# Kernel optimization log

Hardware: AMD Instinct MI355X
Metric: run time of the kernel (lower is better)

## Reference

```python
import jax, jax.numpy as jnp
import numpy as np

B, S, E, H = 4, 2048, 1024, 16
D = E // H  # d_k = 64
NEG = -1000000000.0  # matches torch masked_fill constant


def setup_inputs() -> dict:
    rk = jax.random.key(0)
    kq, kk, kv, km = jax.random.split(rk, 4)
    query = jax.random.normal(kq, (B, S, E), dtype=jnp.float32)
    key = jax.random.normal(kk, (B, S, E), dtype=jnp.float32)
    value = jax.random.normal(kv, (B, S, E), dtype=jnp.float32)
    mask = jax.random.randint(km, (B, S, S), 0, 2, dtype=jnp.int32)
    return {"query": query, "key": key, "value": value, "mask": mask}


def _split_heads(x):
    # (B, S, E) -> (B, H, S, D)
    return x.reshape(B, S, H, D).transpose(0, 2, 1, 3)


def reference(query, key, value, mask):
    q = _split_heads(query)
    k = _split_heads(key)
    v = _split_heads(value)
    scale = np.float32(1.0 / np.sqrt(D))
    scores = jnp.einsum('bhqd,bhkd->bhqk', q, k) * scale  # (B,H,S,S)
    scores = jnp.where(mask[:, None, :, :] == 0, jnp.float32(NEG), scores)
    weights = jax.nn.softmax(scores, axis=-1)
    attn = jnp.einsum('bhqk,bhkd->bhqd', weights, v)  # (B,H,S,D)
    concat = attn.transpose(0, 2, 1, 3).reshape(B, S, E)
    return concat
```

## Files before the change

### kernel.cpp

```cpp
#include <hip/hip_runtime.h>
#include <hip/hip_bf16.h>
#include <math.h>

constexpr int B = 4, S = 2048, E = 1024, H = 16, D = 64;
constexpr float NEGF = -1000000000.0f;
constexpr float KSCALE = 0.125f * 1.44269504f;

typedef __attribute__((ext_vector_type(8))) short short8;
typedef __attribute__((ext_vector_type(16))) float f32x16;

__device__ inline unsigned pk2(float a, float b) {
    unsigned ua = __builtin_bit_cast(unsigned, a) + 0x8000u;
    unsigned ub = __builtin_bit_cast(unsigned, b) + 0x8000u;
    return __builtin_amdgcn_perm(ub, ua, 0x07060302u);
}
__device__ inline void gl_lds16(const void* g, void* l) {
    __builtin_amdgcn_global_load_lds(
        (const __attribute__((address_space(1))) unsigned int*)g,
        (__attribute__((address_space(3))) unsigned int*)l, 16, 0, 0);
}

constexpr size_t WS_K  = 0;
constexpr size_t WS_VT = 18874368;
constexpr size_t WS_MB = 37748736;
constexpr size_t WS_NEED = 54525952;

__global__ void prep_all(const float* __restrict__ K, const float* __restrict__ V,
                         const int* __restrict__ M, char* __restrict__ ws) {
    __shared__ float Vf[64][69];
    const int bid = blockIdx.x, tid = threadIdx.x;

    {
        int g = bid * 256 + tid;
        int rowd = g >> 2, qtr = g & 3;
        int b = rowd >> 15, h = (rowd >> 11) & 15, s = rowd & 2047;
        const float* p = K + ((size_t)(b * S + s)) * E + h * 64 + qtr * 16;
        float4 v0 = *(const float4*)(p + 0),  v1 = *(const float4*)(p + 4);
        float4 v2 = *(const float4*)(p + 8),  v3 = *(const float4*)(p + 12);
        uint4 o0, o1;
        o0.x = pk2(v0.x * KSCALE, v0.y * KSCALE); o0.y = pk2(v0.z * KSCALE, v0.w * KSCALE);
        o0.z = pk2(v1.x * KSCALE, v1.y * KSCALE); o0.w = pk2(v1.z * KSCALE, v1.w * KSCALE);
        o1.x = pk2(v2.x * KSCALE, v2.y * KSCALE); o1.y = pk2(v2.z * KSCALE, v2.w * KSCALE);
        o1.z = pk2(v3.x * KSCALE, v3.y * KSCALE); o1.w = pk2(v3.z * KSCALE, v3.w * KSCALE);
        char* d = ws + WS_K + (size_t)rowd * 144 + qtr * 32;
        *(uint4*)d = o0; *(uint4*)(d + 16) = o1;
        if (qtr == 3) {
            uint4 z; z.x = z.y = z.z = z.w = 0;
            *(uint4*)(d + 32) = z;
        }
    }

    {
        int bh = bid >> 5, kt = bid & 31;
        int b = bh >> 4, h = bh & 15;
        {
            int r = tid >> 2, c4 = (tid & 3) * 16;
            const float* p = V + ((size_t)(b * S + kt * 64 + r)) * E + h * 64 + c4;
            float4 a = *(const float4*)(p + 0), bb = *(const float4*)(p + 4);
            float4 c = *(const float4*)(p + 8), dd = *(const float4*)(p + 12);
            *(float4*)&Vf[r][c4 + 0] = a;  *(float4*)&Vf[r][c4 + 4] = bb;
            *(float4*)&Vf[r][c4 + 8] = c;  *(float4*)&Vf[r][c4 + 12] = dd;
        }
        __syncthreads();
        int d = tid >> 2, sq = (tid & 3) * 16;
        float v[16];
#pragma unroll
        for (int i = 0; i < 16; ++i) v[i] = Vf[sq + i][d];
        uint4 o0, o1;
        o0.x = pk2(v[0], v[1]);   o0.y = pk2(v[2], v[3]);
        o0.z = pk2(v[4], v[5]);   o0.w = pk2(v[6], v[7]);
        o1.x = pk2(v[8], v[9]);   o1.y = pk2(v[10], v[11]);
        o1.z = pk2(v[12], v[13]); o1.w = pk2(v[14], v[15]);
        char* o = ws + WS_VT + ((size_t)(bh * 32 + kt)) * 9216 + d * 144 + sq * 2;
        *(uint4*)o = o0; *(uint4*)(o + 16) = o1;
        if (sq == 48) {
            uint4 z; z.x = z.y = z.z = z.w = 0;
            *(uint4*)(o + 32) = z;
        }
    }

    {
        unsigned* Mb = (unsigned*)(ws + WS_MB);
        const int t = bid * 256 + tid;
#pragma unroll
        for (int it = 0; it < 8; ++it) {
            int gidx = it * 524288 + t;
            int4 mv = *((const int4*)M + gidx);
            unsigned d = (mv.x ? 0xFFu : 0u) | (mv.y ? 0xFF00u : 0u)
                       | (mv.z ? 0xFF0000u : 0u) | (mv.w ? 0xFF000000u : 0u);
            int row = gidx >> 4, g = gidx & 15;
            Mb[row * 16 + (g & 1) * 8 + (g >> 1)] = d;
        }
    }
}

__global__ __launch_bounds__(256, 4)
void fa_mfma(const float* __restrict__ Q, const char* __restrict__ ws,
             float* __restrict__ O) {
    __shared__ char smem[36864];
    const int tid = threadIdx.x;
    const int w = tid >> 6, lane = tid & 63;
    const int L5 = lane & 31, h6 = lane >> 5;
    const int h = blockIdx.x & 15, b = (blockIdx.x >> 4) & 3, qt = blockIdx.x >> 6;
    const int bh = b * 16 + h;
    const int q0w = qt * 128 + w * 32;

    const char* Kws  = ws + WS_K;
    const char* Vtws = ws + WS_VT;
    const int qA = q0w + L5;
    const char* mrow = ws + WS_MB + ((size_t)(b * S + qA)) * 2048 + h6 * 32;

    short8 qf[4];
#pragma unroll
    for (int ks = 0; ks < 4; ++ks) {
        const float* qp = Q + ((size_t)(b * S + qA)) * E + h * 64 + ks * 16 + h6 * 8;
        float4 a = *(const float4*)qp;
        float4 c = *(const float4*)(qp + 4);
        uint4 u;
        u.x = pk2(a.x, a.y); u.y = pk2(a.z, a.w);
        u.z = pk2(c.x, c.y); u.w = pk2(c.z, c.w);
        qf[ks] = *(short8*)&u;
    }

    f32x16 acc[2];
#pragma unroll
    for (int mb = 0; mb < 2; ++mb) acc[mb] = (f32x16)0.0f;
    float l0 = 0.0f;

    {
        const char* ksrc = Kws + ((size_t)bh * S) * 144;
        const char* vsrc = Vtws + ((size_t)bh * 32) * 9216;
#pragma unroll
        for (int c = 0; c < 5; ++c) {
            int idx = c * 4 + w;
            if (idx < 18) {
                int off = idx * 1024;
                const char* g = (off < 9216) ? (ksrc + off) : (vsrc + off - 9216);
                gl_lds16(g + lane * 16, smem + off);
            }
        }
    }

    for (int ti = 0; ti < 32; ++ti) {
        __syncthreads();

        if (ti + 1 < 32) {
            const char* ksrc = Kws + ((size_t)bh * S + (ti + 1) * 64) * 144;
            const char* vsrc = Vtws + ((size_t)(bh * 32 + ti + 1)) * 9216;
            char* dst = smem + ((ti + 1) & 1) * 18432;
#pragma unroll
            for (int c = 0; c < 5; ++c) {
                int idx = c * 4 + w;
                if (idx < 18) {
                    int off = idx * 1024;
                    const char* g = (off < 9216) ? (ksrc + off) : (vsrc + off - 9216);
                    gl_lds16(g + lane * 16, dst + off);
                }
            }
        }
        const uint4 mlo = *(const uint4*)(mrow + ti * 64);
        const uint4 mhi = *(const uint4*)(mrow + ti * 64 + 16);
        const unsigned mdw[8] = {mlo.x, mlo.y, mlo.z, mlo.w,
                                 mhi.x, mhi.y, mhi.z, mhi.w};

        const char* Ks = smem + (ti & 1) * 18432;
        const char* Vt = Ks + 9216;

#pragma unroll
        for (int mbK = 0; mbK < 2; ++mbK) {
            short8 kf[4];
#pragma unroll
            for (int ks = 0; ks < 4; ++ks)
                kf[ks] = *(const short8*)(Ks + (mbK * 32 + L5) * 144 + ks * 32 + h6 * 16);

            f32x16 s = (f32x16)0.0f;
#pragma unroll
            for (int ks = 0; ks < 4; ++ks)
                s = __builtin_amdgcn_mfma_f32_32x32x16_bf16(kf[ks], qf[ks], s, 0, 0, 0);

            float lacc = 0.0f;
            unsigned pd[8];
#pragma unroll
            for (int i = 0; i < 8; ++i) {
                float e0 = __builtin_amdgcn_exp2f(s[2 * i]);
                float e1 = __builtin_amdgcn_exp2f(s[2 * i + 1]);
                unsigned pm = pk2(e0, e1);
                const unsigned mv = mdw[mbK * 4 + (i >> 1)];
                const unsigned am = __builtin_amdgcn_perm(
                    mv, mv, (i & 1) ? 0x03030202u : 0x01010000u);
                pm &= am;
                pd[i] = pm;
                float lo = __builtin_bit_cast(float, pm << 16);
                float hi = __builtin_bit_cast(float, pm & 0xFFFF0000u);
                lacc += lo + hi;
            }
            l0 += lacc;

            short8 pf[2];
#pragma unroll
            for (int sub = 0; sub < 2; ++sub) {
                const unsigned dA = pd[4 * sub + 0], dB = pd[4 * sub + 1];
                const unsigned dC = pd[4 * sub + 2], dD = pd[4 * sub + 3];
                const unsigned t0 = h6 ? dA : dC;
                const unsigned t1 = h6 ? dB : dD;
                const unsigned r0 = (unsigned)__shfl_xor((int)t0, 32, 64);
                const unsigned r1 = (unsigned)__shfl_xor((int)t1, 32, 64);
                uint4 u;
                u.x = h6 ? r0 : dA;  u.y = h6 ? r1 : dB;
                u.z = h6 ? dC : r0;  u.w = h6 ? dD : r1;
                pf[sub] = *(short8*)&u;
            }

#pragma unroll
            for (int mbV = 0; mbV < 2; ++mbV) {
#pragma unroll
                for (int sub = 0; sub < 2; ++sub) {
                    short8 vf = *(const short8*)(Vt + (mbV * 32 + L5) * 144
                                                 + (mbK * 2 + sub) * 32 + h6 * 16);
                    acc[mbV] = __builtin_amdgcn_mfma_f32_32x32x16_bf16(
                        vf, pf[sub], acc[mbV], 0, 0, 0);
                }
            }
        }
    }

    l0 += __shfl_xor(l0, 32, 64);
    const float inv = 1.0f / l0;
    __syncthreads();
    float* ep = (float*)(smem + w * 4608);
#pragma unroll
    for (int mb = 0; mb < 2; ++mb) {
#pragma unroll
        for (int r = 0; r < 16; ++r) {
            const int d = (r & 3) + 8 * (r >> 2) + h6 * 4;
            ep[L5 * 36 + d] = acc[mb][r] * inv;
        }
        __builtin_amdgcn_s_waitcnt(0xc07f);
        const int row = lane >> 1, c = (lane & 1) * 16;
#pragma unroll
        for (int i = 0; i < 4; ++i) {
            float4 t = *(const float4*)&ep[row * 36 + c + 4 * i];
            *(float4*)(O + ((size_t)(b * S + q0w + row)) * E
                         + h * 64 + mb * 32 + c + 4 * i) = t;
        }
        __builtin_amdgcn_s_waitcnt(0xc07f);
    }
}

constexpr int QT = 64, KT = 64, LD = D + 4;
constexpr float SCALE = 0.125f;
__global__ __launch_bounds__(256, 3)
void fa_fp32(const float* __restrict__ Q, const float* __restrict__ K,
             const float* __restrict__ V, const int* __restrict__ M,
             float* __restrict__ Out)
{
    __shared__ float Qs[QT][LD];
    __shared__ float Vs[KT][LD];
    __shared__ float KPs[KT][LD];
    const int tid = threadIdx.x, tx = tid & 15, ty = tid >> 4;
    const int bid = blockIdx.x;
    const int h = bid % H, b = (bid / H) % B, qt = bid / (H * B);
    const int q0 = qt * QT;
    {
        const int col = tx * 4;
#pragma unroll
        for (int i = 0; i < 4; ++i) {
            const int row = ty + i * 16;
            *(float4*)&Qs[row][col] = *(const float4*)&Q[((size_t)(b * S + q0 + row)) * E + h * D + col];
        }
    }
    const int qr0 = ty * 4, d0 = tx * 4;
    float acc[4][4] = {};
    float m_i[4], l_i[4];
#pragma unroll
    for (int j = 0; j < 4; ++j) { m_i[j] = -INFINITY; l_i[j] = 0.0f; }
    for (int kt = 0; kt < S; kt += KT) {
        __syncthreads();
        {
            const int col = tx * 4;
#pragma unroll
            for (int i = 0; i < 4; ++i) {
                const int row = ty + i * 16;
                const size_t g = ((size_t)(b * S + kt + row)) * E + h * D + col;
                *(float4*)&KPs[row][col] = *(const float4*)&K[g];
                *(float4*)&Vs[row][col] = *(const float4*)&V[g];
            }
        }
        __syncthreads();
        float s[4][4] = {};
#pragma unroll
        for (int d = 0; d < D; d += 4) {
            float4 a[4], bb[4];
#pragma unroll
            for (int j = 0; j < 4; ++j) a[j] = *(const float4*)&Qs[qr0 + j][d];
#pragma unroll
            for (int i = 0; i < 4; ++i) bb[i] = *(const float4*)&KPs[tx + 16 * i][d];
#pragma unroll
            for (int j = 0; j < 4; ++j)
#pragma unroll
                for (int i = 0; i < 4; ++i)
                    s[j][i] += a[j].x * bb[i].x + a[j].y * bb[i].y + a[j].z * bb[i].z + a[j].w * bb[i].w;
        }
#pragma unroll
        for (int j = 0; j < 4; ++j) {
            const int* mrow = &M[((size_t)b * S + (q0 + qr0 + j)) * S + kt];
#pragma unroll
            for (int i = 0; i < 4; ++i) {
                const int mk = mrow[tx + 16 * i];
                s[j][i] = mk ? s[j][i] * SCALE : NEGF;
            }
        }
#pragma unroll
        for (int j = 0; j < 4; ++j) {
            float tm = fmaxf(fmaxf(s[j][0], s[j][1]), fmaxf(s[j][2], s[j][3]));
#pragma unroll
            for (int off = 8; off; off >>= 1) tm = fmaxf(tm, __shfl_xor(tm, off, 16));
            const float nm = fmaxf(m_i[j], tm);
            const float alpha = __expf(m_i[j] - nm);
            m_i[j] = nm;
            float rs = 0.0f;
#pragma unroll
            for (int i = 0; i < 4; ++i) { const float p = __expf(s[j][i] - nm); s[j][i] = p; rs += p; }
#pragma unroll
            for (int off = 8; off; off >>= 1) rs += __shfl_xor(rs, off, 16);
            l_i[j] = l_i[j] * alpha + rs;
#pragma unroll
            for (int dd = 0; dd < 4; ++dd) acc[j][dd] *= alpha;
        }
        __syncthreads();
#pragma unroll
        for (int j = 0; j < 4; ++j)
#pragma unroll
            for (int i = 0; i < 4; ++i) KPs[qr0 + j][tx + 16 * i] = s[j][i];
        __syncthreads();
#pragma unroll 4
        for (int kk = 0; kk < KT; kk += 4) {
            float4 p[4], vv[4];
#pragma unroll
            for (int j = 0; j < 4; ++j) p[j] = *(const float4*)&KPs[qr0 + j][kk];
#pragma unroll
            for (int u = 0; u < 4; ++u) vv[u] = *(const float4*)&Vs[kk + u][d0];
#pragma unroll
            for (int j = 0; j < 4; ++j) {
                acc[j][0] += p[j].x * vv[0].x + p[j].y * vv[1].x + p[j].z * vv[2].x + p[j].w * vv[3].x;
                acc[j][1] += p[j].x * vv[0].y + p[j].y * vv[1].y + p[j].z * vv[2].y + p[j].w * vv[3].y;
                acc[j][2] += p[j].x * vv[0].z + p[j].y * vv[1].z + p[j].z * vv[2].z + p[j].w * vv[3].z;
                acc[j][3] += p[j].x * vv[0].w + p[j].y * vv[1].w + p[j].z * vv[2].w + p[j].w * vv[3].w;
            }
        }
    }
#pragma unroll
    for (int j = 0; j < 4; ++j) {
        const float iv = 1.0f / l_i[j];
        float4 r;
        r.x = acc[j][0] * iv; r.y = acc[j][1] * iv; r.z = acc[j][2] * iv; r.w = acc[j][3] * iv;
        *(float4*)&Out[((size_t)(b * S + q0 + qr0 + j)) * E + h * D + d0] = r;
    }
}

extern "C" void kernel_launch(void* const* d_in, const int* in_sizes, int n_in,
                              void* d_out, int out_size, void* d_ws, size_t ws_size,
                              hipStream_t stream) {
    (void)in_sizes; (void)n_in; (void)out_size;
    const float* q = (const float*)d_in[0];
    const float* k = (const float*)d_in[1];
    const float* v = (const float*)d_in[2];
    const int*   m = (const int*)d_in[3];
    float* out = (float*)d_out;

    if (ws_size >= WS_NEED) {
        char* ws = (char*)d_ws;
        prep_all<<<2048, 256, 0, stream>>>(k, v, m, ws);
        fa_mfma<<<1024, 256, 0, stream>>>(q, ws, out);
    } else {
        fa_fp32<<<B * H * (S / QT), 256, 0, stream>>>(q, k, v, m, out);
    }
}
```

Baseline: 300.8 us.

## Double per-wave query rows and route P through LDS instead of shuffles

Each wave now handles 64 query rows (two 32-row blocks), so every K/V tile loaded into LDS is reused across twice as many queries and the grid is halved to 512 blocks. The softmax probabilities are written to a per-wave LDS scratch and read back as MFMA operands, replacing the cross-half-wave shuffles. The K/V double buffer is dropped in favour of a single buffer loaded between two barriers each iteration. This costs some load/compute overlap and lowers occupancy (launch bounds 2, larger LDS) in exchange for better reuse.

```diff
diff --git a/kernel.cpp b/kernel.cpp
--- a/kernel.cpp
+++ b/kernel.cpp
@@ -94,154 +94,158 @@
     }
 }
 
-__global__ __launch_bounds__(256, 4)
+__global__ __launch_bounds__(256, 2)
 void fa_mfma(const float* __restrict__ Q, const char* __restrict__ ws,
              float* __restrict__ O) {
-    __shared__ char smem[36864];
+    __shared__ char smem[55296];
     const int tid = threadIdx.x;
     const int w = tid >> 6, lane = tid & 63;
     const int L5 = lane & 31, h6 = lane >> 5;
     const int h = blockIdx.x & 15, b = (blockIdx.x >> 4) & 3, qt = blockIdx.x >> 6;
     const int bh = b * 16 + h;
-    const int q0w = qt * 128 + w * 32;
+    const int q0w = qt * 256 + w * 64;
+    char* const Ps = smem + 18432 + w * 9216;
 
     const char* Kws  = ws + WS_K;
     const char* Vtws = ws + WS_VT;
-    const int qA = q0w + L5;
-    const char* mrow = ws + WS_MB + ((size_t)(b * S + qA)) * 2048 + h6 * 32;
-
-    short8 qf[4];
-#pragma unroll
-    for (int ks = 0; ks < 4; ++ks) {
-        const float* qp = Q + ((size_t)(b * S + qA)) * E + h * 64 + ks * 16 + h6 * 8;
-        float4 a = *(const float4*)qp;
-        float4 c = *(const float4*)(qp + 4);
-        uint4 u;
-        u.x = pk2(a.x, a.y); u.y = pk2(a.z, a.w);
-        u.z = pk2(c.x, c.y); u.w = pk2(c.z, c.w);
-        qf[ks] = *(short8*)&u;
-    }
-
-    f32x16 acc[2];
-#pragma unroll
-    for (int mb = 0; mb < 2; ++mb) acc[mb] = (f32x16)0.0f;
-    float l0 = 0.0f;
-
-    {
-        const char* ksrc = Kws + ((size_t)bh * S) * 144;
-        const char* vsrc = Vtws + ((size_t)bh * 32) * 9216;
-#pragma unroll
-        for (int c = 0; c < 5; ++c) {
-            int idx = c * 4 + w;
-            if (idx < 18) {
-                int off = idx * 1024;
-                const char* g = (off < 9216) ? (ksrc + off) : (vsrc + off - 9216);
-                gl_lds16(g + lane * 16, smem + off);
-            }
-        }
-    }
+    const int qA = q0w + L5, qB = qA + 32;
+    const char* mrowA = ws + WS_MB + ((size_t)(b * S + qA)) * 2048 + h6 * 32;
+    const char* mrowB = ws + WS_MB + ((size_t)(b * S + qB)) * 2048 + h6 * 32;
+
+    short8 qf[2][4];
+#pragma unroll
+    for (int nb = 0; nb < 2; ++nb)
+#pragma unroll
+        for (int ks = 0; ks < 4; ++ks) {
+            const float* qp = Q + ((size_t)(b * S + q0w + nb * 32 + L5)) * E
+                                + h * 64 + ks * 16 + h6 * 8;
+            float4 a = *(const float4*)qp;
+            float4 c = *(const float4*)(qp + 4);
+            uint4 u;
+            u.x = pk2(a.x, a.y); u.y = pk2(a.z, a.w);
+            u.z = pk2(c.x, c.y); u.w = pk2(c.z, c.w);
+            qf[nb][ks] = *(short8*)&u;
+        }
+
+    f32x16 acc[2][2];
+#pragma unroll
+    for (int mb = 0; mb < 2; ++mb)
+#pragma unroll
+        for (int nb = 0; nb < 2; ++nb) acc[mb][nb] = (f32x16)0.0f;
+    float l0 = 0.0f, l1 = 0.0f;
 
     for (int ti = 0; ti < 32; ++ti) {
-        __syncthreads();
-
-        if (ti + 1 < 32) {
-            const char* ksrc = Kws + ((size_t)bh * S + (ti + 1) * 64) * 144;
-            const char* vsrc = Vtws + ((size_t)(bh * 32 + ti + 1)) * 9216;
-            char* dst = smem + ((ti + 1) & 1) * 18432;
+        const uint4 mAl = *(const uint4*)(mrowA + ti * 64);
+        const uint4 mAh = *(const uint4*)(mrowA + ti * 64 + 16);
+        const uint4 mBl = *(const uint4*)(mrowB + ti * 64);
+        const uint4 mBh = *(const uint4*)(mrowB + ti * 64 + 16);
+        const unsigned mdwA[8] = {mAl.x, mAl.y, mAl.z, mAl.w, mAh.x, mAh.y, mAh.z, mAh.w};
+        const unsigned mdwB[8] = {mBl.x, mBl.y, mBl.z, mBl.w, mBh.x, mBh.y, mBh.z, mBh.w};
+
+        __syncthreads();
+        {
+            const char* ksrc = Kws + ((size_t)bh * S + ti * 64) * 144;
+            const char* vsrc = Vtws + ((size_t)(bh * 32 + ti)) * 9216;
 #pragma unroll
             for (int c = 0; c < 5; ++c) {
                 int idx = c * 4 + w;
                 if (idx < 18) {
                     int off = idx * 1024;
                     const char* g = (off < 9216) ? (ksrc + off) : (vsrc + off - 9216);
-                    gl_lds16(g + lane * 16, dst + off);
+                    gl_lds16(g + lane * 16, smem + off);
                 }
             }
         }
-        const uint4 mlo = *(const uint4*)(mrow + ti * 64);
-        const uint4 mhi = *(const uint4*)(mrow + ti * 64 + 16);
-        const unsigned mdw[8] = {mlo.x, mlo.y, mlo.z, mlo.w,
-                                 mhi.x, mhi.y, mhi.z, mhi.w};
-
-        const char* Ks = smem + (ti & 1) * 18432;
-        const char* Vt = Ks + 9216;
+        __syncthreads();
 
 #pragma unroll
         for (int mbK = 0; mbK < 2; ++mbK) {
             short8 kf[4];
 #pragma unroll
             for (int ks = 0; ks < 4; ++ks)
-                kf[ks] = *(const short8*)(Ks + (mbK * 32 + L5) * 144 + ks * 32 + h6 * 16);
-
-            f32x16 s = (f32x16)0.0f;
+                kf[ks] = *(const short8*)(smem + (mbK * 32 + L5) * 144 + ks * 32 + h6 * 16);
+#pragma unroll
+            for (int nb = 0; nb < 2; ++nb) {
+                f32x16 s = (f32x16)0.0f;
+#pragma unroll
+                for (int ks = 0; ks < 4; ++ks)
+                    s = __builtin_amdgcn_mfma_f32_32x32x16_bf16(kf[ks], qf[nb][ks], s, 0, 0, 0);
+
+                const unsigned* mdw = nb ? mdwB : mdwA;
+                float lacc = 0.0f;
+                unsigned pd[8];
+#pragma unroll
+                for (int i = 0; i < 8; ++i) {
+                    float e0 = __builtin_amdgcn_exp2f(s[2 * i]);
+                    float e1 = __builtin_amdgcn_exp2f(s[2 * i + 1]);
+                    unsigned pm = pk2(e0, e1);
+                    const unsigned mv = mdw[mbK * 4 + (i >> 1)];
+                    const unsigned am = __builtin_amdgcn_perm(
+                        mv, mv, (i & 1) ? 0x03030202u : 0x01010000u);
+                    pm &= am;
+                    pd[i] = pm;
+                    float lo = __builtin_bit_cast(float, pm << 16);
+                    float hi = __builtin_bit_cast(float, pm & 0xFFFF0000u);
+                    lacc += lo + hi;
+                }
+                if (nb) l1 += lacc; else l0 += lacc;
+
+                char* prow = Ps + (nb * 32 + L5) * 144 + mbK * 64 + h6 * 8;
+#pragma unroll
+                for (int g4 = 0; g4 < 4; ++g4) {
+                    uint2 t; t.x = pd[2 * g4]; t.y = pd[2 * g4 + 1];
+                    *(uint2*)(prow + g4 * 16) = t;
+                }
+            }
+        }
+
+        __builtin_amdgcn_s_waitcnt(0xc07f);
+
+        short8 pf[2][4];
+#pragma unroll
+        for (int nb = 0; nb < 2; ++nb)
 #pragma unroll
             for (int ks = 0; ks < 4; ++ks)
-                s = __builtin_amdgcn_mfma_f32_32x32x16_bf16(kf[ks], qf[ks], s, 0, 0, 0);
-
-            float lacc = 0.0f;
-            unsigned pd[8];
-#pragma unroll
-            for (int i = 0; i < 8; ++i) {
-                float e0 = __builtin_amdgcn_exp2f(s[2 * i]);
-                float e1 = __builtin_amdgcn_exp2f(s[2 * i + 1]);
-                unsigned pm = pk2(e0, e1);
-                const unsigned mv = mdw[mbK * 4 + (i >> 1)];
-                const unsigned am = __builtin_amdgcn_perm(
-                    mv, mv, (i & 1) ? 0x03030202u : 0x01010000u);
-                pm &= am;
-                pd[i] = pm;
-                float lo = __builtin_bit_cast(float, pm << 16);
-                float hi = __builtin_bit_cast(float, pm & 0xFFFF0000u);
-                lacc += lo + hi;
-            }
-            l0 += lacc;
-
-            short8 pf[2];
-#pragma unroll
-            for (int sub = 0; sub < 2; ++sub) {
-                const unsigned dA = pd[4 * sub + 0], dB = pd[4 * sub + 1];
-                const unsigned dC = pd[4 * sub + 2], dD = pd[4 * sub + 3];
-                const unsigned t0 = h6 ? dA : dC;
-                const unsigned t1 = h6 ? dB : dD;
-                const unsigned r0 = (unsigned)__shfl_xor((int)t0, 32, 64);
-                const unsigned r1 = (unsigned)__shfl_xor((int)t1, 32, 64);
-                uint4 u;
-                u.x = h6 ? r0 : dA;  u.y = h6 ? r1 : dB;
-                u.z = h6 ? dC : r0;  u.w = h6 ? dD : r1;
-                pf[sub] = *(short8*)&u;
-            }
-
-#pragma unroll
-            for (int mbV = 0; mbV < 2; ++mbV) {
-#pragma unroll
-                for (int sub = 0; sub < 2; ++sub) {
-                    short8 vf = *(const short8*)(Vt + (mbV * 32 + L5) * 144
-                                                 + (mbK * 2 + sub) * 32 + h6 * 16);
-                    acc[mbV] = __builtin_amdgcn_mfma_f32_32x32x16_bf16(
-                        vf, pf[sub], acc[mbV], 0, 0, 0);
-                }
-            }
+                pf[nb][ks] = *(const short8*)(Ps + (nb * 32 + L5) * 144 + ks * 32 + h6 * 16);
+#pragma unroll
+        for (int mbV = 0; mbV < 2; ++mbV) {
+            short8 vf[4];
+#pragma unroll
+            for (int ks = 0; ks < 4; ++ks)
+                vf[ks] = *(const short8*)(smem + 9216 + (mbV * 32 + L5) * 144 + ks * 32 + h6 * 16);
+#pragma unroll
+            for (int nb = 0; nb < 2; ++nb)
+#pragma unroll
+                for (int ks = 0; ks < 4; ++ks)
+                    acc[mbV][nb] = __builtin_amdgcn_mfma_f32_32x32x16_bf16(
+                        vf[ks], pf[nb][ks], acc[mbV][nb], 0, 0, 0);
         }
     }
 
     l0 += __shfl_xor(l0, 32, 64);
-    const float inv = 1.0f / l0;
+    l1 += __shfl_xor(l1, 32, 64);
+    const float inv[2] = {1.0f / l0, 1.0f / l1};
     __syncthreads();
-    float* ep = (float*)(smem + w * 4608);
-#pragma unroll
-    for (int mb = 0; mb < 2; ++mb) {
-#pragma unroll
-        for (int r = 0; r < 16; ++r) {
-            const int d = (r & 3) + 8 * (r >> 2) + h6 * 4;
-            ep[L5 * 36 + d] = acc[mb][r] * inv;
-        }
+#pragma unroll
+    for (int nb = 0; nb < 2; ++nb) {
+#pragma unroll
+        for (int mb = 0; mb < 2; ++mb)
+#pragma unroll
+            for (int g4 = 0; g4 < 4; ++g4) {
+                float4 t;
+                t.x = acc[mb][nb][g4 * 4 + 0] * inv[nb];
+                t.y = acc[mb][nb][g4 * 4 + 1] * inv[nb];
+                t.z = acc[mb][nb][g4 * 4 + 2] * inv[nb];
+                t.w = acc[mb][nb][g4 * 4 + 3] * inv[nb];
+                *(float4*)(Ps + (L5 * 68 + mb * 32 + g4 * 8 + h6 * 4) * 4) = t;
+            }
         __builtin_amdgcn_s_waitcnt(0xc07f);
-        const int row = lane >> 1, c = (lane & 1) * 16;
-#pragma unroll
-        for (int i = 0; i < 4; ++i) {
-            float4 t = *(const float4*)&ep[row * 36 + c + 4 * i];
-            *(float4*)(O + ((size_t)(b * S + q0w + row)) * E
-                         + h * 64 + mb * 32 + c + 4 * i) = t;
+        const int r16 = lane >> 4, dc = lane & 15;
+#pragma unroll
+        for (int i = 0; i < 8; ++i) {
+            const int row = i * 4 + r16;
+            float4 t = *(const float4*)(Ps + (row * 68 + dc * 4) * 4);
+            *(float4*)(O + ((size_t)b * S + q0w + nb * 32 + row) * E + h * 64 + dc * 4) = t;
         }
         __builtin_amdgcn_s_waitcnt(0xc07f);
     }
@@ -371,7 +375,7 @@
     if (ws_size >= WS_NEED) {
         char* ws = (char*)d_ws;
         prep_all<<<2048, 256, 0, stream>>>(k, v, m, ws);
-        fa_mfma<<<1024, 256, 0, stream>>>(q, ws, out);
+        fa_mfma<<<512, 256, 0, stream>>>(q, ws, out);
     } else {
         fa_fp32<<<B * H * (S / QT), 256, 0, stream>>>(q, k, v, m, out);
     }
```

Result: faster. 291.0 us (-3.3%).
